# Optimization experiments

Hardware: AMD Instinct MI355X
Metric: run time of the kernel (lower is better)

Reference implementation:

```python
import jax, jax.numpy as jnp
import numpy as np

FDS = [80, 160, 400, 600]
N, E, G, IN = 20000, 320000, 128, 3072
EPS = 1e-5  # BatchNorm1d default eps


def setup_inputs():
    key = jax.random.key(0)
    ks = iter(jax.random.split(key, 64))
    inp = {}
    inp["x"] = jax.random.normal(next(ks), (N, IN), jnp.float32)
    inp["edge_index"] = jax.random.randint(next(ks), (2, E), 0, N)
    inp["batch"] = jnp.sort(jax.random.randint(next(ks), (N,), 0, G))
    for i, fd in enumerate(FDS):
        din = IN if i == 0 else FDS[i - 1]
        def u(shape, fan):
            s = 1.0 / np.sqrt(fan)
            return jax.random.uniform(next(ks), shape, jnp.float32, -s, s)
        inp[f"wa{i}"] = u((din, 4 * fd), din)      # Linear(din, 4*fd)
        inp[f"ba{i}"] = u((4 * fd,), din)
        inp[f"wb{i}"] = u((4 * fd, fd), 4 * fd)    # Linear(4*fd, fd)
        inp[f"bb{i}"] = u((fd,), 4 * fd)
        inp[f"gw{i}"] = u((fd, fd), fd)            # GCNConv weight
        inp[f"gb{i}"] = jnp.zeros((fd,), jnp.float32)  # GCNConv bias
        inp[f"gamma{i}"] = jnp.ones((fd,), jnp.float32)
        inp[f"beta{i}"] = jnp.zeros((fd,), jnp.float32)
        inp[f"mean{i}"] = jax.random.normal(next(ks), (fd,), jnp.float32) * 0.1
        inp[f"var{i}"] = jax.random.uniform(next(ks), (fd,), jnp.float32, 0.5, 1.5)
    return inp


def _gcn_edges(edge_index, n):
    # GCNConv default: add self-loops, symmetric D^-1/2 (A+I) D^-1/2 normalization
    loops = jnp.arange(n)
    src = jnp.concatenate([edge_index[0], loops])
    dst = jnp.concatenate([edge_index[1], loops])
    deg = jax.ops.segment_sum(jnp.ones(src.shape, jnp.float32), dst, num_segments=n)
    dinv = jnp.where(deg > 0, jax.lax.rsqrt(deg), 0.0)
    return src, dst, dinv[src] * dinv[dst]


def _forward(x, edge_index, batch, params):
    src, dst, norm = _gcn_edges(edge_index, N)
    for (wa, ba, wb, bb, gw, gb, gamma, beta, mean, var) in params:
        h = jax.nn.relu(x @ wa + ba)   # dropout = identity in eval mode
        h = jax.nn.relu(h @ wb + bb)
        h = h @ gw                     # GCN linear transform
        # gather -> normalize -> scatter-add message passing, then bias
        h = jax.ops.segment_sum(h[src] * norm[:, None], dst, num_segments=N) + gb
        # BatchNorm1d (eval: running stats)
        h = (h - mean) * jax.lax.rsqrt(var + EPS) * gamma + beta
        x = jax.nn.relu(h)             # residual branch is dead: dims never match
    return jax.ops.segment_max(x, batch, num_segments=G)  # global_max_pool


def reference(x, edge_index, batch,
              wa0, ba0, wb0, bb0, gw0, gb0, gamma0, beta0, mean0, var0,
              wa1, ba1, wb1, bb1, gw1, gb1, gamma1, beta1, mean1, var1,
              wa2, ba2, wb2, bb2, gw2, gb2, gamma2, beta2, mean2, var2,
              wa3, ba3, wb3, bb3, gw3, gb3, gamma3, beta3, mean3, var3):
    params = [
        (wa0, ba0, wb0, bb0, gw0, gb0, gamma0, beta0, mean0, var0),
        (wa1, ba1, wb1, bb1, gw1, gb1, gamma1, beta1, mean1, var1),
        (wa2, ba2, wb2, bb2, gw2, gb2, gamma2, beta2, mean2, var2),
        (wa3, ba3, wb3, bb3, gw3, gb3, gamma3, beta3, mean3, var3),
    ]
    return _forward(x, edge_index, batch, params)
```

## Files before the change

kernel.cpp:

```cpp
#include <hip/hip_runtime.h>
#include <cstdint>
#include <cstddef>
#include <cmath>


#define EPS_BN 1e-5f

typedef unsigned short u16;
typedef short short8 __attribute__((ext_vector_type(8)));
typedef u16 u16x8 __attribute__((ext_vector_type(8)));
typedef u16 u16x4 __attribute__((ext_vector_type(4)));
typedef float fx4 __attribute__((ext_vector_type(4)));

__device__ __forceinline__ u16 bf16_rn(float f) {
  unsigned u = __float_as_uint(f);
  return (u16)((u + 0x7FFFu + ((u >> 16) & 1u)) >> 16);
}
__device__ __forceinline__ float bf16_f(u16 h) {
  return __uint_as_float(((unsigned)h) << 16);
}

__device__ __forceinline__ void gload16(const void* g, void* l) {
  __builtin_amdgcn_global_load_lds(
      (const __attribute__((address_space(1))) void*)g,
      (__attribute__((address_space(3))) void*)l, 16, 0, 0);
}

#define MEMFENCE() asm volatile("" ::: "memory")

__device__ __forceinline__ void map_tile(int b, int tm, int tn, int T,
                                         int& mt, int& nt) {
  const int x = b & 7;
  const int s = b >> 3;
  const int cap = ((tm - x + 7) >> 3) * tn;
  if (s < cap) {
    const int q = s / tn;
    mt = x + (q << 3);
    nt = s - q * tn;
    return;
  }
  int r = s - cap;
  for (int xp = 0; xp < x; ++xp) {
    const int nbp = (T - xp + 7) >> 3;
    const int capp = ((tm - xp + 7) >> 3) * tn;
    if (nbp > capp) r += nbp - capp;
  }
  for (int xq = 0; xq < 8; ++xq) {
    const int nbq = (T - xq + 7) >> 3;
    const int capq = ((tm - xq + 7) >> 3) * tn;
    const int def = capq - nbq;
    if (def > 0) {
      if (r < def) {
        const int sq = nbq + r;
        const int q = sq / tn;
        mt = xq + (q << 3);
        nt = sq - q * tn;
        return;
      }
      r -= def;
    }
  }
  mt = 0; nt = 0;
}

template <int OUTMODE>
__global__ __launch_bounds__(256, 2) void gemm_ph(
    const u16* __restrict__ Ahi, const u16* __restrict__ Alo,
    const u16* __restrict__ Bhi, const u16* __restrict__ Blo,
    const float* __restrict__ bias,
    float* __restrict__ Cf, u16* __restrict__ Chi, u16* __restrict__ Clo,
    int M, int N, int K, int lda, int ldb, int ldc, int tm, int tn) {
  __shared__ __align__(16) u16 As[2][2][128 * 32];
  __shared__ __align__(16) u16 Bs[2][2][128 * 32];

  int mt, nt;
  map_tile(blockIdx.x, tm, tn, tm * tn, mt, nt);
  const int m0 = mt * 128;
  const int n0 = nt * 128;

  const int tid = threadIdx.x;
  const int lane = tid & 63;
  const int wid = tid >> 6;
  const int wm = (wid >> 1) * 64;
  const int wn = (wid & 1) * 64;
  const int quad = lane >> 4;
  const int l15 = lane & 15;

  const int srow = tid >> 2;
  const int sg = ((tid & 3) ^ srow ^ (srow >> 2)) & 3;
  int ar0 = m0 + srow;      if (ar0 >= M) ar0 = M - 1;
  int ar1 = m0 + srow + 64; if (ar1 >= M) ar1 = M - 1;
  int br0 = n0 + srow;      if (br0 >= N) br0 = N - 1;
  int br1 = n0 + srow + 64; if (br1 >= N) br1 = N - 1;
  const size_t aof0 = (size_t)ar0 * lda + (sg << 3);
  const size_t aof1 = (size_t)ar1 * lda + (sg << 3);
  const size_t bof0 = (size_t)br0 * ldb + (sg << 3);
  const size_t bof1 = (size_t)br1 * ldb + (sg << 3);
  const int l0 = wid << 9;
  const int l1 = 2048 + (wid << 9);

  fx4 zf = {0.f, 0.f, 0.f, 0.f};
  fx4 acc[4][4];
#pragma unroll
  for (int a = 0; a < 4; ++a)
#pragma unroll
    for (int b = 0; b < 4; ++b) acc[a][b] = zf;

  const int nk = (K + 31) >> 5;

  auto stageA = [&](int kt, int bufi) {
    const size_t kk = (size_t)kt << 5;
    gload16(Ahi + aof0 + kk, &As[bufi][0][l0]);
    gload16(Ahi + aof1 + kk, &As[bufi][0][l1]);
    gload16(Alo + aof0 + kk, &As[bufi][1][l0]);
    gload16(Alo + aof1 + kk, &As[bufi][1][l1]);
  };
  auto stageB = [&](int kt, int bufi) {
    const size_t kk = (size_t)kt << 5;
    gload16(Bhi + bof0 + kk, &Bs[bufi][0][l0]);
    gload16(Bhi + bof1 + kk, &Bs[bufi][0][l1]);
    gload16(Blo + bof0 + kk, &Bs[bufi][1][l0]);
    gload16(Blo + bof1 + kk, &Bs[bufi][1][l1]);
  };

  stageA(0, 0); stageB(0, 0);
  if (nk > 1) { stageA(1, 1); stageB(1, 1); }
  if (nk > 1) asm volatile("s_waitcnt vmcnt(8)" ::: "memory");
  else        asm volatile("s_waitcnt vmcnt(0)" ::: "memory");
  __builtin_amdgcn_s_barrier();
  MEMFENCE();

  for (int ki = 0; ki < nk; ++ki) {
    const int cur = ki & 1;
    const bool st = (ki + 2) < nk;

    short8 bh[4], bl[4], ah, al;
#pragma unroll
    for (int t = 0; t < 4; ++t) {
      const int rB = wn + t * 16 + l15;
      const int ob = rB * 32 + (((quad ^ rB ^ (rB >> 2)) & 3) << 3);
      bh[t] = *(const short8*)&Bs[cur][0][ob];
      bl[t] = *(const short8*)&Bs[cur][1][ob];
    }
    {
      const int rA = wm + l15;
      const int oa = rA * 32 + (((quad ^ rA ^ (rA >> 2)) & 3) << 3);
      ah = *(const short8*)&As[cur][0][oa];
      al = *(const short8*)&As[cur][1][oa];
    }
    __builtin_amdgcn_s_setprio(1);
#pragma unroll
    for (int b = 0; b < 4; ++b) {
      acc[0][b] = __builtin_amdgcn_mfma_f32_16x16x32_bf16(ah, bh[b], acc[0][b], 0, 0, 0);
      acc[0][b] = __builtin_amdgcn_mfma_f32_16x16x32_bf16(ah, bl[b], acc[0][b], 0, 0, 0);
      acc[0][b] = __builtin_amdgcn_mfma_f32_16x16x32_bf16(al, bh[b], acc[0][b], 0, 0, 0);
    }
    __builtin_amdgcn_s_setprio(0);
    MEMFENCE();
    __builtin_amdgcn_s_barrier();
    MEMFENCE();

#pragma unroll
    for (int t = 1; t < 4; ++t) {
      const int rA = wm + t * 16 + l15;
      const int oa = rA * 32 + (((quad ^ rA ^ (rA >> 2)) & 3) << 3);
      ah = *(const short8*)&As[cur][0][oa];
      al = *(const short8*)&As[cur][1][oa];
      if (t == 1 && st) {
        stageB(ki + 2, cur);
        if (wid == 0) stageA(ki + 2, cur);
      }
      if (t == 2 && st && wid == 1) stageA(ki + 2, cur);
      if (t == 3 && st && wid == 2) stageA(ki + 2, cur);
      __builtin_amdgcn_s_setprio(1);
#pragma unroll
      for (int b = 0; b < 4; ++b) {
        acc[t][b] = __builtin_amdgcn_mfma_f32_16x16x32_bf16(ah, bh[b], acc[t][b], 0, 0, 0);
        acc[t][b] = __builtin_amdgcn_mfma_f32_16x16x32_bf16(ah, bl[b], acc[t][b], 0, 0, 0);
        acc[t][b] = __builtin_amdgcn_mfma_f32_16x16x32_bf16(al, bh[b], acc[t][b], 0, 0, 0);
      }
      __builtin_amdgcn_s_setprio(0);
      MEMFENCE();
      __builtin_amdgcn_s_barrier();
      MEMFENCE();
    }
    if (st && wid == 3) stageA(ki + 2, cur);
    if (st)                asm volatile("s_waitcnt vmcnt(8)" ::: "memory");
    else if (ki + 1 < nk)  asm volatile("s_waitcnt vmcnt(0)" ::: "memory");
    MEMFENCE();
    __builtin_amdgcn_s_barrier();
    MEMFENCE();
  }

#pragma unroll
  for (int a = 0; a < 4; ++a)
#pragma unroll
    for (int b = 0; b < 4; ++b) {
      const int gn = n0 + wn + b * 16 + l15;
      if (gn >= ldc) continue;
      const bool live = gn < N;
      const float bv = (OUTMODE == 1 && live) ? bias[gn] : 0.f;
#pragma unroll
      for (int r = 0; r < 4; ++r) {
        const int gm = m0 + wm + a * 16 + quad * 4 + r;
        if (gm >= M) continue;
        float v = live ? acc[a][b][r] : 0.f;
        if (OUTMODE == 1) {
          v = live ? fmaxf(v + bv, 0.f) : 0.f;
          const u16 hb = bf16_rn(v);
          Chi[(size_t)gm * ldc + gn] = hb;
          Clo[(size_t)gm * ldc + gn] = bf16_rn(v - bf16_f(hb));
        } else {
          Cf[(size_t)gm * ldc + gn] = v;
        }
      }
    }
}

__global__ __launch_bounds__(256, 2) void gemm_splita(
    const float* __restrict__ Af,
    const u16* __restrict__ Bhi, const u16* __restrict__ Blo,
    const float* __restrict__ bias,
    u16* __restrict__ Chi, u16* __restrict__ Clo,
    int M, int N, int K, int lda, int ldb, int ldc, int tm, int tn) {
  __shared__ __align__(16) u16 As[2][128 * 32];
  __shared__ __align__(16) u16 Bs[2][128 * 32];

  int mt, nt;
  map_tile(blockIdx.x, tm, tn, tm * tn, mt, nt);
  const int m0 = mt * 128;
  const int n0 = nt * 128;

  const int tid = threadIdx.x;
  const int lane = tid & 63;
  const int wid = tid >> 6;
  const int wm = (wid >> 1) * 64;
  const int wn = (wid & 1) * 64;
  const int quad = lane >> 4;
  const int l15 = lane & 15;

  const int srow = tid >> 2;
  const int sg = ((tid & 3) ^ srow ^ (srow >> 2)) & 3;
  int ar0 = m0 + srow;      if (ar0 >= M) ar0 = M - 1;
  int ar1 = m0 + srow + 64; if (ar1 >= M) ar1 = M - 1;
  int br0 = n0 + srow;      if (br0 >= N) br0 = N - 1;
  int br1 = n0 + srow + 64; if (br1 >= N) br1 = N - 1;
  const size_t aof0 = (size_t)ar0 * lda + (sg << 3);
  const size_t aof1 = (size_t)ar1 * lda + (sg << 3);
  const size_t bof0 = (size_t)br0 * ldb + (sg << 3);
  const size_t bof1 = (size_t)br1 * ldb + (sg << 3);
  const int l0 = wid << 9;
  const int l1 = 2048 + (wid << 9);
  const int wls = srow * 32 + ((tid & 3) << 3);

  fx4 zf = {0.f, 0.f, 0.f, 0.f};
  fx4 acc[4][4];
#pragma unroll
  for (int a = 0; a < 4; ++a)
#pragma unroll
    for (int b = 0; b < 4; ++b) acc[a][b] = zf;

  const int nk = (K + 31) >> 5;
  for (int ki = 0; ki < nk; ++ki) {
    const int k0 = ki << 5;
    u16x8 va_h[2], va_l[2];
#pragma unroll
    for (int it = 0; it < 2; ++it) {
      const float* pp = Af + (it ? aof1 : aof0) + k0;
      const fx4 f0 = *(const fx4*)pp;
      const fx4 f1 = *(const fx4*)(pp + 4);
      u16x8 h, l;
#pragma unroll
      for (int j = 0; j < 4; ++j) {
        const u16 hb = bf16_rn(f0[j]);
        h[j] = hb;
        l[j] = bf16_rn(f0[j] - bf16_f(hb));
      }
#pragma unroll
      for (int j = 0; j < 4; ++j) {
        const u16 hb = bf16_rn(f1[j]);
        h[4 + j] = hb;
        l[4 + j] = bf16_rn(f1[j] - bf16_f(hb));
      }
      va_h[it] = h;
      va_l[it] = l;
    }

    if (ki) __syncthreads();

    gload16(Bhi + bof0 + k0, &Bs[0][l0]);
    gload16(Bhi + bof1 + k0, &Bs[0][l1]);
    gload16(Blo + bof0 + k0, &Bs[1][l0]);
    gload16(Blo + bof1 + k0, &Bs[1][l1]);
    *(u16x8*)&As[0][wls] = va_h[0];
    *(u16x8*)&As[0][wls + 2048] = va_h[1];
    *(u16x8*)&As[1][wls] = va_l[0];
    *(u16x8*)&As[1][wls + 2048] = va_l[1];
    __syncthreads();

    short8 ah[4], al[4], bh[4], bl[4];
#pragma unroll
    for (int t = 0; t < 4; ++t) {
      const int rA = wm + t * 16 + l15;
      const int oa = rA * 32 + (((quad ^ rA ^ (rA >> 2)) & 3) << 3);
      ah[t] = *(const short8*)&As[0][oa];
      al[t] = *(const short8*)&As[1][oa];
      const int rB = wn + t * 16 + l15;
      const int ob = rB * 32 + (((quad ^ rB ^ (rB >> 2)) & 3) << 3);
      bh[t] = *(const short8*)&Bs[0][ob];
      bl[t] = *(const short8*)&Bs[1][ob];
    }
#pragma unroll
    for (int a = 0; a < 4; ++a)
#pragma unroll
      for (int b = 0; b < 4; ++b) {
        acc[a][b] = __builtin_amdgcn_mfma_f32_16x16x32_bf16(ah[a], bh[b], acc[a][b], 0, 0, 0);
        acc[a][b] = __builtin_amdgcn_mfma_f32_16x16x32_bf16(ah[a], bl[b], acc[a][b], 0, 0, 0);
        acc[a][b] = __builtin_amdgcn_mfma_f32_16x16x32_bf16(al[a], bh[b], acc[a][b], 0, 0, 0);
      }
  }

#pragma unroll
  for (int a = 0; a < 4; ++a)
#pragma unroll
    for (int b = 0; b < 4; ++b) {
      const int gn = n0 + wn + b * 16 + l15;
      if (gn >= ldc) continue;
      const bool live = gn < N;
      const float bv = live ? bias[gn] : 0.f;
#pragma unroll
      for (int r = 0; r < 4; ++r) {
        const int gm = m0 + wm + a * 16 + quad * 4 + r;
        if (gm < M) {
          float v = live ? fmaxf(acc[a][b][r] + bv, 0.f) : 0.f;
          const u16 hb = bf16_rn(v);
          Chi[(size_t)gm * ldc + gn] = hb;
          Clo[(size_t)gm * ldc + gn] = bf16_rn(v - bf16_f(hb));
        }
      }
    }
}

struct TSJob { const float* W; u16* Th; u16* Tl; int K; int Kp; int N; int tiles_k; int base; };
struct TSJobs { TSJob j[12]; };

__global__ __launch_bounds__(256) void transpose_split_all(TSJobs jobs, int njobs) {
  const int b = blockIdx.x;
  int ji = 0;
  while (ji + 1 < njobs && jobs.j[ji + 1].base <= b) ++ji;
  const TSJob J = jobs.j[ji];
  const int t = b - J.base;
  const int k0 = (t % J.tiles_k) * 32;
  const int n0 = (t / J.tiles_k) * 32;
  __shared__ float tile[32][33];
  const int tx = threadIdx.x & 31, ty = threadIdx.x >> 5;
#pragma unroll
  for (int i = 0; i < 32; i += 8) {
    const int k = k0 + ty + i, n = n0 + tx;
    tile[ty + i][tx] = (k < J.K && n < J.N) ? J.W[(size_t)k * J.N + n] : 0.f;
  }
  __syncthreads();
#pragma unroll
  for (int i = 0; i < 32; i += 8) {
    const int n = n0 + ty + i, k = k0 + tx;
    if (n < J.N && k < J.Kp) {
      const float f = tile[tx][ty + i];
      const u16 hb = bf16_rn(f);
      J.Th[(size_t)n * J.Kp + k] = hb;
      J.Tl[(size_t)n * J.Kp + k] = bf16_rn(f - bf16_f(hb));
    }
  }
}

__global__ void count_deg(const int* __restrict__ dst, int E, int* __restrict__ cnt) {
  int e = blockIdx.x * blockDim.x + threadIdx.x;
  if (e < E) atomicAdd(&cnt[dst[e]], 1);
}

__global__ void compute_dinv(const int* __restrict__ cnt, float* __restrict__ dinv, int N) {
  int i = blockIdx.x * blockDim.x + threadIdx.x;
  if (i < N) dinv[i] = rsqrtf((float)(cnt[i] + 1));
}

__global__ void scan_block(const int* __restrict__ cnt, int* __restrict__ partial,
                           int* __restrict__ blocksum, int N) {
  __shared__ int s[256];
  const int t = threadIdx.x;
  const int i = blockIdx.x * 256 + t;
  int v = (i < N) ? cnt[i] : 0;
  s[t] = v;
  __syncthreads();
  for (int off = 1; off < 256; off <<= 1) {
    int u = (t >= off) ? s[t - off] : 0;
    __syncthreads();
    s[t] += u;
    __syncthreads();
  }
  if (i < N) partial[i] = s[t];
  if (t == 255) blocksum[blockIdx.x] = s[255];
}

__global__ void scan_sums(int* __restrict__ blocksum, int NB) {
  __shared__ int s[256];
  const int t = threadIdx.x;
  int v = (t < NB) ? blocksum[t] : 0;
  s[t] = v;
  __syncthreads();
  for (int off = 1; off < 256; off <<= 1) {
    int u = (t >= off) ? s[t - off] : 0;
    __syncthreads();
    s[t] += u;
    __syncthreads();
  }
  if (t < NB) blocksum[t] = s[t] - v;
}

__global__ void finalize_rowptr(const int* __restrict__ partial, const int* __restrict__ blockoff,
                                int* __restrict__ rowptr, int N) {
  int i = blockIdx.x * 256 + threadIdx.x;
  if (i < N) rowptr[i + 1] = partial[i] + blockoff[blockIdx.x];
  if (i == 0) rowptr[0] = 0;
}

__global__ void fill_csr(const int* __restrict__ src, const int* __restrict__ dst, int E,
                         const int* __restrict__ rowptr, int* __restrict__ cursor,
                         int* __restrict__ colidx) {
  int e = blockIdx.x * blockDim.x + threadIdx.x;
  if (e < E) {
    int d = dst[e];
    int p = atomicAdd(&cursor[d], 1);
    colidx[rowptr[d] + p] = src[e];
  }
}

__global__ void mp_bn_relu(
    const float* __restrict__ H, const int* __restrict__ rowptr,
    const int* __restrict__ colidx, const float* __restrict__ dinv,
    const float* __restrict__ gb, const float* __restrict__ gamma,
    const float* __restrict__ beta, const float* __restrict__ mean,
    const float* __restrict__ var,
    u16* __restrict__ Xh, u16* __restrict__ Xl, int N, int F, int Fp) {
  const int nch = Fp >> 2;
  const int idx = blockIdx.x * blockDim.x + threadIdx.x;
  if (idx >= N * nch) return;
  const int i = idx / nch;
  const int c = idx - i * nch;
  const size_t rowi = (size_t)i * Fp + (c << 2);
  if ((c << 2) >= F) {
    const u16x4 z = {0, 0, 0, 0};
    *(u16x4*)(Xh + rowi) = z;
    *(u16x4*)(Xl + rowi) = z;
    return;
  }
  const float di = dinv[i];
  fx4 acc = (di * di) * *(const fx4*)(H + rowi);
  const int e0 = rowptr[i], e1 = rowptr[i + 1];
  int e = e0;
  for (; e + 4 <= e1; e += 4) {
    const int s0 = colidx[e + 0], s1 = colidx[e + 1];
    const int s2 = colidx[e + 2], s3 = colidx[e + 3];
    const float w0 = di * dinv[s0], w1 = di * dinv[s1];
    const float w2 = di * dinv[s2], w3 = di * dinv[s3];
    const fx4 v0 = *(const fx4*)(H + (size_t)s0 * Fp + (c << 2));
    const fx4 v1 = *(const fx4*)(H + (size_t)s1 * Fp + (c << 2));
    const fx4 v2 = *(const fx4*)(H + (size_t)s2 * Fp + (c << 2));
    const fx4 v3 = *(const fx4*)(H + (size_t)s3 * Fp + (c << 2));
    acc += w0 * v0;
    acc += w1 * v1;
    acc += w2 * v2;
    acc += w3 * v3;
  }
  for (; e < e1; ++e) {
    const int s = colidx[e];
    acc += (di * dinv[s]) * *(const fx4*)(H + (size_t)s * Fp + (c << 2));
  }
  u16x4 oh, ol;
#pragma unroll
  for (int j = 0; j < 4; ++j) {
    const int col = (c << 2) + j;
    float v = (acc[j] + gb[col] - mean[col]) * rsqrtf(var[col] + EPS_BN) * gamma[col] + beta[col];
    v = fmaxf(v, 0.f);
    const u16 hb = bf16_rn(v);
    oh[j] = hb;
    ol[j] = bf16_rn(v - bf16_f(hb));
  }
  *(u16x4*)(Xh + rowi) = oh;
  *(u16x4*)(Xl + rowi) = ol;
}

__global__ void pool_seg(const u16* __restrict__ Xh, const u16* __restrict__ Xl,
                         const int* __restrict__ batch, float* __restrict__ out,
                         int N, int F, int ldx) {
  const int g = blockIdx.x;
  int lo = 0, hi = N;
  while (lo < hi) { int m = (lo + hi) >> 1; if (batch[m] < g) lo = m + 1; else hi = m; }
  const int s0 = lo;
  hi = N;
  while (lo < hi) { int m = (lo + hi) >> 1; if (batch[m] <= g) lo = m + 1; else hi = m; }
  const int s1 = lo;
  const int c = threadIdx.x;
  if (c * 4 >= F) return;
  fx4 mx = {-INFINITY, -INFINITY, -INFINITY, -INFINITY};
  for (int i = s0; i < s1; ++i) {
    const size_t off = (size_t)i * ldx + (c << 2);
    const u16x4 h = *(const u16x4*)(Xh + off);
    const u16x4 l = *(const u16x4*)(Xl + off);
#pragma unroll
    for (int j = 0; j < 4; ++j) mx[j] = fmaxf(mx[j], bf16_f(h[j]) + bf16_f(l[j]));
  }
  *(fx4*)(out + (size_t)g * F + (c << 2)) = mx;
}

extern "C" void kernel_launch(void* const* d_in, const int* in_sizes, int n_in,
                              void* d_out, int out_size, void* d_ws, size_t ws_size,
                              hipStream_t stream) {
  const float* x = (const float*)d_in[0];
  const int* edges = (const int*)d_in[1];
  const int* batch = (const int*)d_in[2];
  const int E = in_sizes[1] / 2;
  const int Nn = in_sizes[2];

  static const int FDS[4]  = {80, 160, 400, 600};
  static const int FDP[4]  = {96, 160, 416, 608};
  static const int DINS[4] = {3072, 80, 160, 400};
  static const int DINP[4] = {3072, 96, 160, 416};
  const float *wa[4], *ba[4], *wb[4], *bb[4], *gw[4], *gb[4], *gamma[4], *beta[4], *mean[4], *var[4];
  for (int i = 0; i < 4; ++i) {
    const int b = 3 + 10 * i;
    wa[i] = (const float*)d_in[b + 0];
    ba[i] = (const float*)d_in[b + 1];
    wb[i] = (const float*)d_in[b + 2];
    bb[i] = (const float*)d_in[b + 3];
    gw[i] = (const float*)d_in[b + 4];
    gb[i] = (const float*)d_in[b + 5];
    gamma[i] = (const float*)d_in[b + 6];
    beta[i] = (const float*)d_in[b + 7];
    mean[i] = (const float*)d_in[b + 8];
    var[i] = (const float*)d_in[b + 9];
  }

  char* p = (char*)d_ws;
  auto alloc = [&](size_t bytes) {
    char* r = p;
    p += (bytes + 255) & ~(size_t)255;
    return r;
  };
  u16* actA_h = (u16*)alloc((size_t)Nn * 2400 * 2);
  u16* actA_l = (u16*)alloc((size_t)Nn * 2400 * 2);
  u16* actB_h = (u16*)alloc((size_t)Nn * 608 * 2);
  u16* actB_l = (u16*)alloc((size_t)Nn * 608 * 2);
  float* H3 = (float*)actA_h;

  u16 *waT_h[4], *waT_l[4], *wbT_h[4], *wbT_l[4], *gwT_h[4], *gwT_l[4];
  for (int i = 0; i < 4; ++i) {
    const size_t s1 = (size_t)4 * FDS[i] * DINP[i];
    const size_t s2 = (size_t)FDS[i] * 4 * FDS[i];
    const size_t s3 = (size_t)FDS[i] * FDP[i];
    waT_h[i] = (u16*)alloc(s1 * 2);
    waT_l[i] = (u16*)alloc(s1 * 2);
    wbT_h[i] = (u16*)alloc(s2 * 2);
    wbT_l[i] = (u16*)alloc(s2 * 2);
    gwT_h[i] = (u16*)alloc(s3 * 2);
    gwT_l[i] = (u16*)alloc(s3 * 2);
  }

  int* cnt = (int*)alloc((size_t)Nn * sizeof(int));
  int* cursor = (int*)alloc((size_t)Nn * sizeof(int));
  int* partial = (int*)alloc((size_t)Nn * sizeof(int));
  int* blocksum = (int*)alloc(256 * sizeof(int));
  int* rowptr = (int*)alloc((size_t)(Nn + 1) * sizeof(int));
  int* colidx = (int*)alloc((size_t)E * sizeof(int));
  float* dinv = (float*)alloc((size_t)Nn * sizeof(float));

  const int* srcIdx = edges;
  const int* dstIdx = edges + E;

  {
    TSJobs jobs;
    int base = 0, ji = 0;
    auto addjob = [&](const float* W, int K, int Kp, int Ncols, u16* Th, u16* Tl) {
      const int tk = Kp / 32, tn = (Ncols + 31) / 32;
      jobs.j[ji++] = TSJob{W, Th, Tl, K, Kp, Ncols, tk, base};
      base += tk * tn;
    };
    for (int i = 0; i < 4; ++i) {
      addjob(wa[i], DINS[i], DINP[i], 4 * FDS[i], waT_h[i], waT_l[i]);
      addjob(wb[i], 4 * FDS[i], 4 * FDS[i], FDS[i], wbT_h[i], wbT_l[i]);
      addjob(gw[i], FDS[i], FDP[i], FDS[i], gwT_h[i], gwT_l[i]);
    }
    transpose_split_all<<<base, 256, 0, stream>>>(jobs, 12);
  }

  hipMemsetAsync(cnt, 0, (size_t)Nn * sizeof(int), stream);
  hipMemsetAsync(cursor, 0, (size_t)Nn * sizeof(int), stream);

  const int EB = (E + 255) / 256;
  const int NB = (Nn + 255) / 256;
  count_deg<<<EB, 256, 0, stream>>>(dstIdx, E, cnt);
  compute_dinv<<<NB, 256, 0, stream>>>(cnt, dinv, Nn);
  scan_block<<<NB, 256, 0, stream>>>(cnt, partial, blocksum, Nn);
  scan_sums<<<1, 256, 0, stream>>>(blocksum, NB);
  finalize_rowptr<<<NB, 256, 0, stream>>>(partial, blocksum, rowptr, Nn);
  fill_csr<<<EB, 256, 0, stream>>>(srcIdx, dstIdx, E, rowptr, cursor, colidx);

  const int tm = (Nn + 127) / 128;
  for (int i = 0; i < 4; ++i) {
    const int fd = FDS[i], fdp = FDP[i];
    const int hid = 4 * fd;
    const int din = DINS[i], dinp = DINP[i];

    {
      const int tn = (hid + 127) / 128;
      if (i == 0) {
        gemm_splita<<<tm * tn, 256, 0, stream>>>(
            x, waT_h[0], waT_l[0], ba[0],
            actA_h, actA_l, Nn, hid, din, din, dinp, hid, tm, tn);
      } else {
        gemm_ph<1><<<tm * tn, 256, 0, stream>>>(
            actB_h, actB_l, waT_h[i], waT_l[i], ba[i],
            nullptr, actA_h, actA_l, Nn, hid, din, dinp, dinp, hid, tm, tn);
      }
    }
    {
      const int tn = (fd + 127) / 128;
      gemm_ph<1><<<tm * tn, 256, 0, stream>>>(
          actA_h, actA_l, wbT_h[i], wbT_l[i], bb[i],
          nullptr, actB_h, actB_l, Nn, fd, hid, hid, hid, fdp, tm, tn);
    }
    {
      const int tn = (fd + 127) / 128;
      gemm_ph<0><<<tm * tn, 256, 0, stream>>>(
          actB_h, actB_l, gwT_h[i], gwT_l[i], nullptr,
          H3, nullptr, nullptr, Nn, fd, fd, fdp, fdp, fdp, tm, tn);
    }
    {
      const int items = Nn * (fdp >> 2);
      mp_bn_relu<<<(items + 255) / 256, 256, 0, stream>>>(
          H3, rowptr, colidx, dinv, gb[i], gamma[i], beta[i], mean[i], var[i],
          actB_h, actB_l, Nn, fd, fdp);
    }
  }

  pool_seg<<<out_size / 600, 192, 0, stream>>>(actB_h, actB_l, batch, (float*)d_out,
                                               Nn, 600, 608);
}
```

Baseline: 1.850 ms.

## Simplify GEMM main loop to a single-barrier double-buffered prefetch

Replaces the hand-scheduled GEMM K-loop, which prefetched two tiles ahead and staggered the A-tile loads across waves between four barrier-separated MFMA groups. The new loop does one __syncthreads per K step, then issues the next tile's async global-to-LDS loads into the other buffer. It then reads all A and B fragments at once and runs all 48 MFMAs back to back. This removes three barriers and the priority toggling per K step, in exchange for shallower prefetch (one tile ahead), no explicit vmcnt control, and more live fragment registers.

```diff
diff --git a/kernel.cpp b/kernel.cpp
--- a/kernel.cpp
+++ b/kernel.cpp
@@ -25,8 +25,6 @@
       (const __attribute__((address_space(1))) void*)g,
       (__attribute__((address_space(3))) void*)l, 16, 0, 0);
 }
-
-#define MEMFENCE() asm volatile("" ::: "memory")
 
 __device__ __forceinline__ void map_tile(int b, int tm, int tn, int T,
                                          int& mt, int& nt) {
@@ -108,88 +106,51 @@
 
   const int nk = (K + 31) >> 5;
 
-  auto stageA = [&](int kt, int bufi) {
-    const size_t kk = (size_t)kt << 5;
-    gload16(Ahi + aof0 + kk, &As[bufi][0][l0]);
-    gload16(Ahi + aof1 + kk, &As[bufi][0][l1]);
-    gload16(Alo + aof0 + kk, &As[bufi][1][l0]);
-    gload16(Alo + aof1 + kk, &As[bufi][1][l1]);
-  };
-  auto stageB = [&](int kt, int bufi) {
-    const size_t kk = (size_t)kt << 5;
-    gload16(Bhi + bof0 + kk, &Bs[bufi][0][l0]);
-    gload16(Bhi + bof1 + kk, &Bs[bufi][0][l1]);
-    gload16(Blo + bof0 + kk, &Bs[bufi][1][l0]);
-    gload16(Blo + bof1 + kk, &Bs[bufi][1][l1]);
-  };
-
-  stageA(0, 0); stageB(0, 0);
-  if (nk > 1) { stageA(1, 1); stageB(1, 1); }
-  if (nk > 1) asm volatile("s_waitcnt vmcnt(8)" ::: "memory");
-  else        asm volatile("s_waitcnt vmcnt(0)" ::: "memory");
-  __builtin_amdgcn_s_barrier();
-  MEMFENCE();
+  gload16(Ahi + aof0, &As[0][0][l0]);
+  gload16(Ahi + aof1, &As[0][0][l1]);
+  gload16(Alo + aof0, &As[0][1][l0]);
+  gload16(Alo + aof1, &As[0][1][l1]);
+  gload16(Bhi + bof0, &Bs[0][0][l0]);
+  gload16(Bhi + bof1, &Bs[0][0][l1]);
+  gload16(Blo + bof0, &Bs[0][1][l0]);
+  gload16(Blo + bof1, &Bs[0][1][l1]);
 
   for (int ki = 0; ki < nk; ++ki) {
     const int cur = ki & 1;
-    const bool st = (ki + 2) < nk;
-
-    short8 bh[4], bl[4], ah, al;
+    __syncthreads();
+
+    if (ki + 1 < nk) {
+      const size_t kn = (size_t)(ki + 1) << 5;
+      gload16(Ahi + aof0 + kn, &As[cur ^ 1][0][l0]);
+      gload16(Ahi + aof1 + kn, &As[cur ^ 1][0][l1]);
+      gload16(Alo + aof0 + kn, &As[cur ^ 1][1][l0]);
+      gload16(Alo + aof1 + kn, &As[cur ^ 1][1][l1]);
+      gload16(Bhi + bof0 + kn, &Bs[cur ^ 1][0][l0]);
+      gload16(Bhi + bof1 + kn, &Bs[cur ^ 1][0][l1]);
+      gload16(Blo + bof0 + kn, &Bs[cur ^ 1][1][l0]);
+      gload16(Blo + bof1 + kn, &Bs[cur ^ 1][1][l1]);
+    }
+
+    short8 ah[4], al[4], bh[4], bl[4];
 #pragma unroll
     for (int t = 0; t < 4; ++t) {
+      const int rA = wm + t * 16 + l15;
+      const int oa = rA * 32 + (((quad ^ rA ^ (rA >> 2)) & 3) << 3);
+      ah[t] = *(const short8*)&As[cur][0][oa];
+      al[t] = *(const short8*)&As[cur][1][oa];
       const int rB = wn + t * 16 + l15;
       const int ob = rB * 32 + (((quad ^ rB ^ (rB >> 2)) & 3) << 3);
       bh[t] = *(const short8*)&Bs[cur][0][ob];
       bl[t] = *(const short8*)&Bs[cur][1][ob];
     }
-    {
-      const int rA = wm + l15;
-      const int oa = rA * 32 + (((quad ^ rA ^ (rA >> 2)) & 3) << 3);
-      ah = *(const short8*)&As[cur][0][oa];
-      al = *(const short8*)&As[cur][1][oa];
-    }
-    __builtin_amdgcn_s_setprio(1);
-#pragma unroll
-    for (int b = 0; b < 4; ++b) {
-      acc[0][b] = __builtin_amdgcn_mfma_f32_16x16x32_bf16(ah, bh[b], acc[0][b], 0, 0, 0);
-      acc[0][b] = __builtin_amdgcn_mfma_f32_16x16x32_bf16(ah, bl[b], acc[0][b], 0, 0, 0);
-      acc[0][b] = __builtin_amdgcn_mfma_f32_16x16x32_bf16(al, bh[b], acc[0][b], 0, 0, 0);
-    }
-    __builtin_amdgcn_s_setprio(0);
-    MEMFENCE();
-    __builtin_amdgcn_s_barrier();
-    MEMFENCE();
-
-#pragma unroll
-    for (int t = 1; t < 4; ++t) {
-      const int rA = wm + t * 16 + l15;
-      const int oa = rA * 32 + (((quad ^ rA ^ (rA >> 2)) & 3) << 3);
-      ah = *(const short8*)&As[cur][0][oa];
-      al = *(const short8*)&As[cur][1][oa];
-      if (t == 1 && st) {
-        stageB(ki + 2, cur);
-        if (wid == 0) stageA(ki + 2, cur);
-      }
-      if (t == 2 && st && wid == 1) stageA(ki + 2, cur);
-      if (t == 3 && st && wid == 2) stageA(ki + 2, cur);
-      __builtin_amdgcn_s_setprio(1);
+#pragma unroll
+    for (int a = 0; a < 4; ++a)
 #pragma unroll
       for (int b = 0; b < 4; ++b) {
-        acc[t][b] = __builtin_amdgcn_mfma_f32_16x16x32_bf16(ah, bh[b], acc[t][b], 0, 0, 0);
-        acc[t][b] = __builtin_amdgcn_mfma_f32_16x16x32_bf16(ah, bl[b], acc[t][b], 0, 0, 0);
-        acc[t][b] = __builtin_amdgcn_mfma_f32_16x16x32_bf16(al, bh[b], acc[t][b], 0, 0, 0);
-      }
-      __builtin_amdgcn_s_setprio(0);
-      MEMFENCE();
-      __builtin_amdgcn_s_barrier();
-      MEMFENCE();
-    }
-    if (st && wid == 3) stageA(ki + 2, cur);
-    if (st)                asm volatile("s_waitcnt vmcnt(8)" ::: "memory");
-    else if (ki + 1 < nk)  asm volatile("s_waitcnt vmcnt(0)" ::: "memory");
-    MEMFENCE();
-    __builtin_amdgcn_s_barrier();
-    MEMFENCE();
+        acc[a][b] = __builtin_amdgcn_mfma_f32_16x16x32_bf16(ah[a], bh[b], acc[a][b], 0, 0, 0);
+        acc[a][b] = __builtin_amdgcn_mfma_f32_16x16x32_bf16(ah[a], bl[b], acc[a][b], 0, 0, 0);
+        acc[a][b] = __builtin_amdgcn_mfma_f32_16x16x32_bf16(al[a], bh[b], acc[a][b], 0, 0, 0);
+      }
   }
 
 #pragma unroll
```

Result: faster. 1.794 ms (-3.1%).
